# Performance work log

Measured on AMD Instinct MI355X. Metric: run time of the kernel, lower is better.

The kernel has to match this reference:

```python
import jax, jax.numpy as jnp
import numpy as np

N, E = 8192, 65536
IN_C, OUT_C, EF = 64, 16, 8
L1, L2 = 48, 32  # in - floor((in-out)/3), in - floor(2*(in-out)/3)


def setup_inputs() -> dict:
    key = jax.random.key(0)
    ks = jax.random.split(key, 10)
    rn = lambda k, shape, s: jax.random.normal(k, shape, dtype=jnp.float32) * s
    return {
        "x": jax.random.normal(ks[0], (N, IN_C), dtype=jnp.float32),
        "edge_index": jax.random.randint(ks[1], (2, E), 0, N, dtype=jnp.int32),
        "edge_attr": jax.random.normal(ks[2], (E, EF), dtype=jnp.float32),
        "nn1_w": rn(ks[3], (EF, IN_C * L1), 0.05),
        "nn1_b": jnp.zeros((IN_C * L1,), jnp.float32),
        "root1": rn(ks[4], (IN_C, L1), 0.1),
        "bias1": jnp.zeros((L1,), jnp.float32),
        "nn2_w": rn(ks[5], (EF, L1 * L2), 0.05),
        "nn2_b": jnp.zeros((L1 * L2,), jnp.float32),
        "root2": rn(ks[6], (L1, L2), 0.1),
        "bias2": jnp.zeros((L2,), jnp.float32),
        "mu_w": rn(ks[7], (L2, OUT_C), 0.1),
        "mu_b": jnp.zeros((OUT_C,), jnp.float32),
        "ls_w": rn(ks[8], (L2, OUT_C), 0.1),
        "ls_b": jnp.zeros((OUT_C,), jnp.float32),
    }


def _nnconv(x, src, dst, edge_attr, nn_w, nn_b, root, bias, c_in, c_out):
    # edge MLP -> per-edge weight matrices [E, c_in, c_out]
    w = (edge_attr @ nn_w + nn_b).reshape(-1, c_in, c_out)
    msg = jnp.einsum('ei,eio->eo', x[src], w)  # gather + per-edge matvec
    agg = jax.ops.segment_sum(msg, dst, num_segments=x.shape[0])  # sum aggregation
    return agg + x @ root + bias  # root transform + bias


def _gcn(x, src, dst, w, b):
    n = x.shape[0]
    # degree over target nodes, including self-loop (edge_weight = 1)
    deg = jax.ops.segment_sum(jnp.ones_like(src, jnp.float32), dst, num_segments=n) + 1.0
    dinv = jax.lax.rsqrt(deg)
    h = x @ w
    norm = dinv[src] * dinv[dst]  # [E]
    agg = jax.ops.segment_sum(h[src] * norm[:, None], dst, num_segments=n)
    return agg + h * (1.0 / deg)[:, None] + b  # self-loop contribution: deg_i^{-1}


def reference(x, edge_index, edge_attr, nn1_w, nn1_b, root1, bias1,
              nn2_w, nn2_b, root2, bias2, mu_w, mu_b, ls_w, ls_b):
    src, dst = edge_index[0], edge_index[1]
    h = jax.nn.relu(_nnconv(x, src, dst, edge_attr, nn1_w, nn1_b, root1, bias1, IN_C, L1))
    h = jax.nn.relu(_nnconv(h, src, dst, edge_attr, nn2_w, nn2_b, root2, bias2, L1, L2))
    return (_gcn(h, src, dst, mu_w, mu_b), _gcn(h, src, dst, ls_w, ls_b))
```

## Files before the change

kernel.cpp:

```cpp
#include <hip/hip_runtime.h>

#define NN 8192
#define EE 65536
#define K1 640
#define K2 480
#define ZS1 652
#define ZS2 492


__global__ __launch_bounds__(256) void k_zero(int* __restrict__ p) {
    int i = blockIdx.x * 256 + threadIdx.x;
    ((int4*)p)[i] = make_int4(0, 0, 0, 0);
}

__global__ __launch_bounds__(256) void k_count(const int* __restrict__ ei,
                                               int* __restrict__ cnt) {
    int e = blockIdx.x * 256 + threadIdx.x;
    if (e < EE) atomicAdd(&cnt[ei[EE + e]], 1);
}

__global__ __launch_bounds__(256) void k_scan(const int* __restrict__ cnt,
                                              int* __restrict__ rowstart,
                                              int* __restrict__ cursor) {
    __shared__ int part[256];
    const int t = threadIdx.x;
    const int base = t * 32;
    int local[32];
    int sum = 0;
#pragma unroll
    for (int k = 0; k < 32; k++) { local[k] = cnt[base + k]; sum += local[k]; }
    part[t] = sum;
    __syncthreads();
    if (t == 0) {
        int run = 0;
        for (int i = 0; i < 256; i++) { int c = part[i]; part[i] = run; run += c; }
    }
    __syncthreads();
    int run = part[t];
#pragma unroll
    for (int k = 0; k < 32; k++) {
        rowstart[base + k] = run;
        cursor[base + k] = run;
        run += local[k];
    }
    if (t == 255) rowstart[NN] = run;
}

__global__ __launch_bounds__(256) void k_scatter(const int* __restrict__ ei,
                                                 const float* __restrict__ ea,
                                                 int* __restrict__ cursor,
                                                 int* __restrict__ ssrc,
                                                 float* __restrict__ sea) {
    int e = blockIdx.x * 256 + threadIdx.x;
    if (e >= EE) return;
    int s = ei[e], d = ei[EE + e];
    int pos = atomicAdd(&cursor[d], 1);
    ssrc[pos] = s;
    const float4* a = (const float4*)(ea + (size_t)e * 8);
    float4* bp = (float4*)(sea + (size_t)pos * 8);
    bp[0] = a[0];
    bp[1] = a[1];
}

__global__ __launch_bounds__(256) void k_L1(const int* __restrict__ rowstart,
                                            const int* __restrict__ ssrc,
                                            const float* __restrict__ sea,
                                            const float* __restrict__ x,
                                            const float* __restrict__ nn1_w,
                                            const float* __restrict__ nn1_b,
                                            const float* __restrict__ root1,
                                            const float* __restrict__ bias1,
                                            float* __restrict__ h1) {
    __shared__ __align__(16) float Zt[8 * ZS1];
    __shared__ __align__(16) float Ws[64 * 48];
    __shared__ float pacc[8][8][48];
    const int n0 = blockIdx.x * 8;
    {
        const int wv = threadIdx.x >> 6;
        const int i = threadIdx.x & 63;
        const int nnA = wv * 2, nnB = nnA + 1;
        int jA = rowstart[n0 + nnA], eA = rowstart[n0 + nnA + 1];
        int jB = rowstart[n0 + nnB], eB = rowstart[n0 + nnB + 1];
        float aA[8] = {0, 0, 0, 0, 0, 0, 0, 0}, sA = 0.f;
        float aB[8] = {0, 0, 0, 0, 0, 0, 0, 0}, sB = 0.f;
        while (jA < eA || jB < eB) {
            int cjA[8], cjB[8];
#pragma unroll
            for (int p = 0; p < 8; p++) {
                int ja = jA + p; cjA[p] = (ja < eA) ? ja : 0;
                int jb = jB + p; cjB[p] = (jb < eB) ? jb : 0;
            }
            int sjA[8], sjB[8];
#pragma unroll
            for (int p = 0; p < 8; p++) { sjA[p] = ssrc[cjA[p]]; sjB[p] = ssrc[cjB[p]]; }
            float xvA[8], xvB[8];
#pragma unroll
            for (int p = 0; p < 8; p++) {
                xvA[p] = x[(size_t)sjA[p] * 64 + i];
                xvB[p] = x[(size_t)sjB[p] * 64 + i];
            }
#pragma unroll
            for (int p = 0; p < 8; p++) {
                {
                    const float4* q4 = (const float4*)(sea + (size_t)cjA[p] * 8);
                    float4 e0 = q4[0], e1 = q4[1];
                    float xx = (jA + p < eA) ? xvA[p] : 0.f;
                    aA[0] += e0.x * xx; aA[1] += e0.y * xx; aA[2] += e0.z * xx; aA[3] += e0.w * xx;
                    aA[4] += e1.x * xx; aA[5] += e1.y * xx; aA[6] += e1.z * xx; aA[7] += e1.w * xx;
                    sA += xx;
                }
                {
                    const float4* q4 = (const float4*)(sea + (size_t)cjB[p] * 8);
                    float4 e0 = q4[0], e1 = q4[1];
                    float xx = (jB + p < eB) ? xvB[p] : 0.f;
                    aB[0] += e0.x * xx; aB[1] += e0.y * xx; aB[2] += e0.z * xx; aB[3] += e0.w * xx;
                    aB[4] += e1.x * xx; aB[5] += e1.y * xx; aB[6] += e1.z * xx; aB[7] += e1.w * xx;
                    sB += xx;
                }
            }
            jA += 8; jB += 8;
        }
        float* zrA = Zt + nnA * ZS1;
        float* zrB = Zt + nnB * ZS1;
#pragma unroll
        for (int f = 0; f < 8; f++) { zrA[f * 64 + i] = aA[f]; zrB[f * 64 + i] = aB[f]; }
        zrA[512 + i] = sA; zrB[512 + i] = sB;
        zrA[576 + i] = x[(size_t)(n0 + nnA) * 64 + i];
        zrB[576 + i] = x[(size_t)(n0 + nnB) * 64 + i];
    }
    const int o  = threadIdx.x & 15;
    const int q  = (threadIdx.x >> 4) & 1;
    const int ks = threadIdx.x >> 5;
    float acc[4][3];
#pragma unroll
    for (int m = 0; m < 4; m++)
#pragma unroll
        for (int cc = 0; cc < 3; cc++) acc[m][cc] = 0.f;
    for (int c = 0; c < 10; ++c) {
        __syncthreads();
        const float* src = (c < 8) ? nn1_w + c * 3072 : (c == 8 ? nn1_b : root1);
#pragma unroll
        for (int i2 = 0; i2 < 3; i2++) {
            int g = threadIdx.x + i2 * 256;
            *(float4*)&Ws[g * 4] = *(const float4*)&src[g * 4];
        }
        __syncthreads();
        const int kl0 = ks * 8;
        const int kg0 = c * 64 + kl0;
#pragma unroll
        for (int kk = 0; kk < 8; kk += 4) {
            const int kl = kl0 + kk, kg = kg0 + kk;
            float zc[4][4];
#pragma unroll
            for (int m = 0; m < 4; m++) {
                float4 z = *(const float4*)&Zt[(q * 4 + m) * ZS1 + kg];
                zc[m][0] = z.x; zc[m][1] = z.y; zc[m][2] = z.z; zc[m][3] = z.w;
            }
#pragma unroll
            for (int dk = 0; dk < 4; dk++) {
                float w0 = Ws[(kl + dk) * 48 + o];
                float w1 = Ws[(kl + dk) * 48 + o + 16];
                float w2 = Ws[(kl + dk) * 48 + o + 32];
#pragma unroll
                for (int m = 0; m < 4; m++) {
                    acc[m][0] += zc[m][dk] * w0;
                    acc[m][1] += zc[m][dk] * w1;
                    acc[m][2] += zc[m][dk] * w2;
                }
            }
        }
    }
#pragma unroll
    for (int m = 0; m < 4; m++) {
        pacc[ks][q * 4 + m][o]      = acc[m][0];
        pacc[ks][q * 4 + m][o + 16] = acc[m][1];
        pacc[ks][q * 4 + m][o + 32] = acc[m][2];
    }
    __syncthreads();
    for (int r = threadIdx.x; r < 8 * 48; r += 256) {
        int nn = r / 48, oc = r - nn * 48;
        float v = bias1[oc];
#pragma unroll
        for (int k = 0; k < 8; k++) v += pacc[k][nn][oc];
        h1[(size_t)(n0 + nn) * 48 + oc] = v > 0.f ? v : 0.f;
    }
}

__global__ __launch_bounds__(256) void k_L2(const int* __restrict__ rowstart,
                                            const int* __restrict__ ssrc,
                                            const float* __restrict__ sea,
                                            const float* __restrict__ h1,
                                            const float* __restrict__ nn2_w,
                                            const float* __restrict__ nn2_b,
                                            const float* __restrict__ root2,
                                            const float* __restrict__ bias2,
                                            const float* __restrict__ mu_w,
                                            const float* __restrict__ mu_b,
                                            const float* __restrict__ ls_w,
                                            const float* __restrict__ ls_b,
                                            float* __restrict__ hmu,
                                            float* __restrict__ hls,
                                            float* __restrict__ dinv,
                                            float* __restrict__ out) {
    __shared__ __align__(16) float Zt[8 * ZS2];
    __shared__ __align__(16) float Ws[96 * 32];
    __shared__ float pacc[8][8][32];
    __shared__ float h2s[8][33];
    const int n0 = blockIdx.x * 8;
    {
        const int wv = threadIdx.x >> 6;
        const int i = threadIdx.x & 63;
        if (i < 48) {
            const int nnA = wv * 2, nnB = nnA + 1;
            int jA = rowstart[n0 + nnA], eA = rowstart[n0 + nnA + 1];
            int jB = rowstart[n0 + nnB], eB = rowstart[n0 + nnB + 1];
            float aA[8] = {0, 0, 0, 0, 0, 0, 0, 0}, sA = 0.f;
            float aB[8] = {0, 0, 0, 0, 0, 0, 0, 0}, sB = 0.f;
            while (jA < eA || jB < eB) {
                int cjA[8], cjB[8];
#pragma unroll
                for (int p = 0; p < 8; p++) {
                    int ja = jA + p; cjA[p] = (ja < eA) ? ja : 0;
                    int jb = jB + p; cjB[p] = (jb < eB) ? jb : 0;
                }
                int sjA[8], sjB[8];
#pragma unroll
                for (int p = 0; p < 8; p++) { sjA[p] = ssrc[cjA[p]]; sjB[p] = ssrc[cjB[p]]; }
                float hvA[8], hvB[8];
#pragma unroll
                for (int p = 0; p < 8; p++) {
                    hvA[p] = h1[(size_t)sjA[p] * 48 + i];
                    hvB[p] = h1[(size_t)sjB[p] * 48 + i];
                }
#pragma unroll
                for (int p = 0; p < 8; p++) {
                    {
                        const float4* q4 = (const float4*)(sea + (size_t)cjA[p] * 8);
                        float4 e0 = q4[0], e1 = q4[1];
                        float xx = (jA + p < eA) ? hvA[p] : 0.f;
                        aA[0] += e0.x * xx; aA[1] += e0.y * xx; aA[2] += e0.z * xx; aA[3] += e0.w * xx;
                        aA[4] += e1.x * xx; aA[5] += e1.y * xx; aA[6] += e1.z * xx; aA[7] += e1.w * xx;
                        sA += xx;
                    }
                    {
                        const float4* q4 = (const float4*)(sea + (size_t)cjB[p] * 8);
                        float4 e0 = q4[0], e1 = q4[1];
                        float xx = (jB + p < eB) ? hvB[p] : 0.f;
                        aB[0] += e0.x * xx; aB[1] += e0.y * xx; aB[2] += e0.z * xx; aB[3] += e0.w * xx;
                        aB[4] += e1.x * xx; aB[5] += e1.y * xx; aB[6] += e1.z * xx; aB[7] += e1.w * xx;
                        sB += xx;
                    }
                }
                jA += 8; jB += 8;
            }
            float* zrA = Zt + nnA * ZS2;
            float* zrB = Zt + nnB * ZS2;
#pragma unroll
            for (int f = 0; f < 8; f++) { zrA[f * 48 + i] = aA[f]; zrB[f * 48 + i] = aB[f]; }
            zrA[384 + i] = sA; zrB[384 + i] = sB;
            zrA[432 + i] = h1[(size_t)(n0 + nnA) * 48 + i];
            zrB[432 + i] = h1[(size_t)(n0 + nnB) * 48 + i];
        }
    }
    const int o  = threadIdx.x & 15;
    const int q  = (threadIdx.x >> 4) & 1;
    const int ks = threadIdx.x >> 5;
    float acc[4][2];
#pragma unroll
    for (int m = 0; m < 4; m++) { acc[m][0] = 0.f; acc[m][1] = 0.f; }
    for (int c = 0; c < 5; ++c) {
        __syncthreads();
#pragma unroll
        for (int i2 = 0; i2 < 3; i2++) {
            int g = threadIdx.x + i2 * 256;
            const float* s4;
            if (c < 4)          s4 = nn2_w + c * 3072 + g * 4;
            else if (g < 384)   s4 = nn2_b + g * 4;
            else                s4 = root2 + (g - 384) * 4;
            *(float4*)&Ws[g * 4] = *(const float4*)s4;
        }
        __syncthreads();
        const int kl0 = ks * 12;
        const int kg0 = c * 96 + kl0;
#pragma unroll
        for (int kk = 0; kk < 12; kk += 4) {
            const int kl = kl0 + kk, kg = kg0 + kk;
            float zc[4][4];
#pragma unroll
            for (int m = 0; m < 4; m++) {
                float4 z = *(const float4*)&Zt[(q * 4 + m) * ZS2 + kg];
                zc[m][0] = z.x; zc[m][1] = z.y; zc[m][2] = z.z; zc[m][3] = z.w;
            }
#pragma unroll
            for (int dk = 0; dk < 4; dk++) {
                float w0 = Ws[(kl + dk) * 32 + o];
                float w1 = Ws[(kl + dk) * 32 + o + 16];
#pragma unroll
                for (int m = 0; m < 4; m++) {
                    acc[m][0] += zc[m][dk] * w0;
                    acc[m][1] += zc[m][dk] * w1;
                }
            }
        }
    }
#pragma unroll
    for (int m = 0; m < 4; m++) {
        pacc[ks][q * 4 + m][o]      = acc[m][0];
        pacc[ks][q * 4 + m][o + 16] = acc[m][1];
    }
    __syncthreads();
    {
        int nn = threadIdx.x >> 5, oc = threadIdx.x & 31;
        float v = bias2[oc];
#pragma unroll
        for (int k = 0; k < 8; k++) v += pacc[k][nn][oc];
        h2s[nn][oc] = v > 0.f ? v : 0.f;
    }
    __syncthreads();
    if (threadIdx.x < 128) {
        const int oc = threadIdx.x & 15;
        const int nn = threadIdx.x >> 4;
        const int gn = n0 + nn;
        float am = 0.f, al = 0.f;
#pragma unroll
        for (int i = 0; i < 32; i++) {
            float hv = h2s[nn][i];
            am += hv * mu_w[i * 16 + oc];
            al += hv * ls_w[i * 16 + oc];
        }
        float d = (float)(rowstart[gn + 1] - rowstart[gn]) + 1.0f;
        float di = rsqrtf(d);
        if (oc == 0) dinv[gn] = di;
        hmu[(size_t)gn * 16 + oc] = am;
        hls[(size_t)gn * 16 + oc] = al;
        out[(size_t)gn * 16 + oc] = am / d + mu_b[oc];
        out[(size_t)NN * 16 + (size_t)gn * 16 + oc] = al / d + ls_b[oc];
    }
}

__global__ __launch_bounds__(256) void k_gcn(const int* __restrict__ rowstart,
                                             const int* __restrict__ ssrc,
                                             const float* __restrict__ hmu,
                                             const float* __restrict__ hls,
                                             const float* __restrict__ dinv,
                                             float* __restrict__ out) {
    const int wave = threadIdx.x >> 6;
    const int lane = threadIdx.x & 63;
    const int o = lane & 15, p = lane >> 4;
    const int d = blockIdx.x * 4 + wave;
    const int rs = rowstart[d], re = rowstart[d + 1];
    float am = 0.f, al = 0.f;
    for (int j = rs + p; j < re; j += 4) {
        int s = ssrc[j];
        float ds_ = dinv[s];
        am += hmu[(size_t)s * 16 + o] * ds_;
        al += hls[(size_t)s * 16 + o] * ds_;
    }
    am += __shfl_xor(am, 16); al += __shfl_xor(al, 16);
    am += __shfl_xor(am, 32); al += __shfl_xor(al, 32);
    if (p == 0) {
        float dd = dinv[d];
        out[(size_t)d * 16 + o] += am * dd;
        out[(size_t)NN * 16 + (size_t)d * 16 + o] += al * dd;
    }
}

extern "C" void kernel_launch(void* const* d_in, const int* in_sizes, int n_in,
                              void* d_out, int out_size, void* d_ws, size_t ws_size,
                              hipStream_t stream) {
    const float* x     = (const float*)d_in[0];
    const int*   ei    = (const int*)d_in[1];
    const float* ea    = (const float*)d_in[2];
    const float* nn1_w = (const float*)d_in[3];
    const float* nn1_b = (const float*)d_in[4];
    const float* root1 = (const float*)d_in[5];
    const float* bias1 = (const float*)d_in[6];
    const float* nn2_w = (const float*)d_in[7];
    const float* nn2_b = (const float*)d_in[8];
    const float* root2 = (const float*)d_in[9];
    const float* bias2 = (const float*)d_in[10];
    const float* mu_w  = (const float*)d_in[11];
    const float* mu_b  = (const float*)d_in[12];
    const float* ls_w  = (const float*)d_in[13];
    const float* ls_b  = (const float*)d_in[14];
    float* out = (float*)d_out;

    float* W    = (float*)d_ws;
    float* sea  = W;
    float* h1   = sea + 524288;
    float* hmu  = h1 + 393216;
    float* hls  = hmu + 131072;
    float* dinv = hls + 131072;
    int* cnt      = (int*)(dinv + 8192);
    int* rowstart = cnt + 8192;
    int* cursor   = rowstart + 8193;
    int* ssrc     = cursor + 8192;

    k_zero<<<dim3(8), dim3(256), 0, stream>>>(cnt);
    k_count<<<dim3(EE / 256), dim3(256), 0, stream>>>(ei, cnt);
    k_scan<<<dim3(1), dim3(256), 0, stream>>>(cnt, rowstart, cursor);
    k_scatter<<<dim3(EE / 256), dim3(256), 0, stream>>>(ei, ea, cursor, ssrc, sea);
    k_L1<<<dim3(NN / 8), dim3(256), 0, stream>>>(rowstart, ssrc, sea, x,
                                                 nn1_w, nn1_b, root1, bias1, h1);
    k_L2<<<dim3(NN / 8), dim3(256), 0, stream>>>(rowstart, ssrc, sea, h1,
                                                 nn2_w, nn2_b, root2, bias2,
                                                 mu_w, mu_b, ls_w, ls_b,
                                                 hmu, hls, dinv, out);
    k_gcn<<<dim3(NN / 4), dim3(256), 0, stream>>>(rowstart, ssrc,
                                                  hmu, hls, dinv, out);
}
```

Before: 154.6 us.

## Fuse all stages into one persistent cooperative kernel with grid syncs

Replaces the seven separate kernel launches (zero, count, scan, scatter, layer1, layer2, gcn) with a single cooperative persistent kernel. Stages are separated by grid.sync and loop over node tiles with a grid sized from occupancy. Shared memory is merged into one reused buffer, and the GCN stage now maps 8 nodes per block with 2 edge lanes per output. The aim is to remove launch overhead and inter-kernel gaps. In exchange it adds grid-wide barrier costs, runs the serial scan on a single block while the others wait, and may lower occupancy in the heavy layer stages.

After: 536.7 us. 3.47x slower.

```diff
diff --git a/kernel.cpp b/kernel.cpp
--- a/kernel.cpp
+++ b/kernel.cpp
@@ -1,367 +1,363 @@
 #include <hip/hip_runtime.h>
+#include <hip/hip_cooperative_groups.h>
+
+namespace cg = cooperative_groups;
 
 #define NN 8192
 #define EE 65536
-#define K1 640
-#define K2 480
+#define NTILE 1024
 #define ZS1 652
 #define ZS2 492
-
-
-__global__ __launch_bounds__(256) void k_zero(int* __restrict__ p) {
-    int i = blockIdx.x * 256 + threadIdx.x;
-    ((int4*)p)[i] = make_int4(0, 0, 0, 0);
-}
-
-__global__ __launch_bounds__(256) void k_count(const int* __restrict__ ei,
-                                               int* __restrict__ cnt) {
-    int e = blockIdx.x * 256 + threadIdx.x;
-    if (e < EE) atomicAdd(&cnt[ei[EE + e]], 1);
-}
-
-__global__ __launch_bounds__(256) void k_scan(const int* __restrict__ cnt,
-                                              int* __restrict__ rowstart,
-                                              int* __restrict__ cursor) {
-    __shared__ int part[256];
-    const int t = threadIdx.x;
-    const int base = t * 32;
-    int local[32];
-    int sum = 0;
-#pragma unroll
-    for (int k = 0; k < 32; k++) { local[k] = cnt[base + k]; sum += local[k]; }
-    part[t] = sum;
-    __syncthreads();
-    if (t == 0) {
-        int run = 0;
-        for (int i = 0; i < 256; i++) { int c = part[i]; part[i] = run; run += c; }
-    }
-    __syncthreads();
-    int run = part[t];
-#pragma unroll
-    for (int k = 0; k < 32; k++) {
-        rowstart[base + k] = run;
-        cursor[base + k] = run;
-        run += local[k];
-    }
-    if (t == 255) rowstart[NN] = run;
-}
-
-__global__ __launch_bounds__(256) void k_scatter(const int* __restrict__ ei,
-                                                 const float* __restrict__ ea,
-                                                 int* __restrict__ cursor,
-                                                 int* __restrict__ ssrc,
-                                                 float* __restrict__ sea) {
-    int e = blockIdx.x * 256 + threadIdx.x;
-    if (e >= EE) return;
-    int s = ei[e], d = ei[EE + e];
-    int pos = atomicAdd(&cursor[d], 1);
-    ssrc[pos] = s;
-    const float4* a = (const float4*)(ea + (size_t)e * 8);
-    float4* bp = (float4*)(sea + (size_t)pos * 8);
-    bp[0] = a[0];
-    bp[1] = a[1];
-}
-
-__global__ __launch_bounds__(256) void k_L1(const int* __restrict__ rowstart,
-                                            const int* __restrict__ ssrc,
-                                            const float* __restrict__ sea,
-                                            const float* __restrict__ x,
-                                            const float* __restrict__ nn1_w,
-                                            const float* __restrict__ nn1_b,
-                                            const float* __restrict__ root1,
-                                            const float* __restrict__ bias1,
-                                            float* __restrict__ h1) {
-    __shared__ __align__(16) float Zt[8 * ZS1];
-    __shared__ __align__(16) float Ws[64 * 48];
-    __shared__ float pacc[8][8][48];
-    const int n0 = blockIdx.x * 8;
+#define U_OFF 5216
+#define SMEM_FLOATS (U_OFF + 3072)
+
+__global__ __launch_bounds__(256, 4) void k_all(
+    const float* __restrict__ x, const int* __restrict__ ei,
+    const float* __restrict__ ea,
+    const float* __restrict__ nn1_w, const float* __restrict__ nn1_b,
+    const float* __restrict__ root1, const float* __restrict__ bias1,
+    const float* __restrict__ nn2_w, const float* __restrict__ nn2_b,
+    const float* __restrict__ root2, const float* __restrict__ bias2,
+    const float* __restrict__ mu_w, const float* __restrict__ mu_b,
+    const float* __restrict__ ls_w, const float* __restrict__ ls_b,
+    float* out, float* ws) {
+    cg::grid_group grid = cg::this_grid();
+    __shared__ __align__(16) float smem[SMEM_FLOATS];
+
+    float* sea  = ws;
+    float* h1   = sea + 524288;
+    float* hmu  = h1 + 393216;
+    float* hls  = hmu + 131072;
+    float* dinv = hls + 131072;
+    int* cnt      = (int*)(dinv + 8192);
+    int* rowstart = cnt + 8192;
+    int* cursor   = rowstart + 8193;
+    int* ssrc     = cursor + 8192;
+
+    const int tid = blockIdx.x * 256 + threadIdx.x;
+    const int nthreads = gridDim.x * 256;
+
+    for (int i = tid; i < 2048; i += nthreads)
+        ((int4*)cnt)[i] = make_int4(0, 0, 0, 0);
+    grid.sync();
+
+    for (int e = tid; e < EE; e += nthreads)
+        atomicAdd(&cnt[ei[EE + e]], 1);
+    grid.sync();
+
+    if (blockIdx.x == 0) {
+        int* part = (int*)smem;
+        const int t = threadIdx.x;
+        const int base = t * 32;
+        int local[32];
+        int sum = 0;
+#pragma unroll
+        for (int k = 0; k < 32; k++) { local[k] = cnt[base + k]; sum += local[k]; }
+        part[t] = sum;
+        __syncthreads();
+        if (t == 0) {
+            int run = 0;
+            for (int i = 0; i < 256; i++) { int c = part[i]; part[i] = run; run += c; }
+        }
+        __syncthreads();
+        int run = part[t];
+#pragma unroll
+        for (int k = 0; k < 32; k++) {
+            rowstart[base + k] = run;
+            cursor[base + k] = run;
+            run += local[k];
+        }
+        if (t == 255) rowstart[NN] = run;
+    }
+    grid.sync();
+
+    for (int e = tid; e < EE; e += nthreads) {
+        int s = ei[e], d = ei[EE + e];
+        int pos = atomicAdd(&cursor[d], 1);
+        ssrc[pos] = s;
+        const float4* a = (const float4*)(ea + (size_t)e * 8);
+        float4* bp = (float4*)(sea + (size_t)pos * 8);
+        bp[0] = a[0];
+        bp[1] = a[1];
+    }
+    grid.sync();
+
     {
-        const int wv = threadIdx.x >> 6;
-        const int i = threadIdx.x & 63;
-        const int nnA = wv * 2, nnB = nnA + 1;
-        int jA = rowstart[n0 + nnA], eA = rowstart[n0 + nnA + 1];
-        int jB = rowstart[n0 + nnB], eB = rowstart[n0 + nnB + 1];
-        float aA[8] = {0, 0, 0, 0, 0, 0, 0, 0}, sA = 0.f;
-        float aB[8] = {0, 0, 0, 0, 0, 0, 0, 0}, sB = 0.f;
-        while (jA < eA || jB < eB) {
-            int cjA[8], cjB[8];
-#pragma unroll
-            for (int p = 0; p < 8; p++) {
-                int ja = jA + p; cjA[p] = (ja < eA) ? ja : 0;
-                int jb = jB + p; cjB[p] = (jb < eB) ? jb : 0;
-            }
-            int sjA[8], sjB[8];
-#pragma unroll
-            for (int p = 0; p < 8; p++) { sjA[p] = ssrc[cjA[p]]; sjB[p] = ssrc[cjB[p]]; }
-            float xvA[8], xvB[8];
-#pragma unroll
-            for (int p = 0; p < 8; p++) {
-                xvA[p] = x[(size_t)sjA[p] * 64 + i];
-                xvB[p] = x[(size_t)sjB[p] * 64 + i];
-            }
-#pragma unroll
-            for (int p = 0; p < 8; p++) {
-                {
-                    const float4* q4 = (const float4*)(sea + (size_t)cjA[p] * 8);
-                    float4 e0 = q4[0], e1 = q4[1];
-                    float xx = (jA + p < eA) ? xvA[p] : 0.f;
-                    aA[0] += e0.x * xx; aA[1] += e0.y * xx; aA[2] += e0.z * xx; aA[3] += e0.w * xx;
-                    aA[4] += e1.x * xx; aA[5] += e1.y * xx; aA[6] += e1.z * xx; aA[7] += e1.w * xx;
-                    sA += xx;
-                }
-                {
-                    const float4* q4 = (const float4*)(sea + (size_t)cjB[p] * 8);
-                    float4 e0 = q4[0], e1 = q4[1];
-                    float xx = (jB + p < eB) ? xvB[p] : 0.f;
-                    aB[0] += e0.x * xx; aB[1] += e0.y * xx; aB[2] += e0.z * xx; aB[3] += e0.w * xx;
-                    aB[4] += e1.x * xx; aB[5] += e1.y * xx; aB[6] += e1.z * xx; aB[7] += e1.w * xx;
-                    sB += xx;
-                }
-            }
-            jA += 8; jB += 8;
-        }
-        float* zrA = Zt + nnA * ZS1;
-        float* zrB = Zt + nnB * ZS1;
-#pragma unroll
-        for (int f = 0; f < 8; f++) { zrA[f * 64 + i] = aA[f]; zrB[f * 64 + i] = aB[f]; }
-        zrA[512 + i] = sA; zrB[512 + i] = sB;
-        zrA[576 + i] = x[(size_t)(n0 + nnA) * 64 + i];
-        zrB[576 + i] = x[(size_t)(n0 + nnB) * 64 + i];
-    }
-    const int o  = threadIdx.x & 15;
-    const int q  = (threadIdx.x >> 4) & 1;
-    const int ks = threadIdx.x >> 5;
-    float acc[4][3];
-#pragma unroll
-    for (int m = 0; m < 4; m++)
-#pragma unroll
-        for (int cc = 0; cc < 3; cc++) acc[m][cc] = 0.f;
-    for (int c = 0; c < 10; ++c) {
-        __syncthreads();
-        const float* src = (c < 8) ? nn1_w + c * 3072 : (c == 8 ? nn1_b : root1);
-#pragma unroll
-        for (int i2 = 0; i2 < 3; i2++) {
-            int g = threadIdx.x + i2 * 256;
-            *(float4*)&Ws[g * 4] = *(const float4*)&src[g * 4];
-        }
-        __syncthreads();
-        const int kl0 = ks * 8;
-        const int kg0 = c * 64 + kl0;
-#pragma unroll
-        for (int kk = 0; kk < 8; kk += 4) {
-            const int kl = kl0 + kk, kg = kg0 + kk;
-            float zc[4][4];
+        float* Zt = smem;
+        float* U  = smem + U_OFF;
+        for (int tile = blockIdx.x; tile < NTILE; tile += gridDim.x) {
+            const int n0 = tile * 8;
+            {
+                const int wv = threadIdx.x >> 6;
+                const int i = threadIdx.x & 63;
+                const int nnA = wv * 2, nnB = nnA + 1;
+                int jA = rowstart[n0 + nnA], eA = rowstart[n0 + nnA + 1];
+                int jB = rowstart[n0 + nnB], eB = rowstart[n0 + nnB + 1];
+                float aA[8] = {0, 0, 0, 0, 0, 0, 0, 0}, sA = 0.f;
+                float aB[8] = {0, 0, 0, 0, 0, 0, 0, 0}, sB = 0.f;
+                while (jA < eA || jB < eB) {
+                    int cjA[8], cjB[8];
+#pragma unroll
+                    for (int p = 0; p < 8; p++) {
+                        int ja = jA + p; cjA[p] = (ja < eA) ? ja : 0;
+                        int jb = jB + p; cjB[p] = (jb < eB) ? jb : 0;
+                    }
+                    int sjA[8], sjB[8];
+#pragma unroll
+                    for (int p = 0; p < 8; p++) { sjA[p] = ssrc[cjA[p]]; sjB[p] = ssrc[cjB[p]]; }
+                    float xvA[8], xvB[8];
+#pragma unroll
+                    for (int p = 0; p < 8; p++) {
+                        xvA[p] = x[(size_t)sjA[p] * 64 + i];
+                        xvB[p] = x[(size_t)sjB[p] * 64 + i];
+                    }
+#pragma unroll
+                    for (int p = 0; p < 8; p++) {
+                        {
+                            const float4* q4 = (const float4*)(sea + (size_t)cjA[p] * 8);
+                            float4 e0 = q4[0], e1 = q4[1];
+                            float xx = (jA + p < eA) ? xvA[p] : 0.f;
+                            aA[0] += e0.x * xx; aA[1] += e0.y * xx; aA[2] += e0.z * xx; aA[3] += e0.w * xx;
+                            aA[4] += e1.x * xx; aA[5] += e1.y * xx; aA[6] += e1.z * xx; aA[7] += e1.w * xx;
+                            sA += xx;
+                        }
+                        {
+                            const float4* q4 = (const float4*)(sea + (size_t)cjB[p] * 8);
+                            float4 e0 = q4[0], e1 = q4[1];
+                            float xx = (jB + p < eB) ? xvB[p] : 0.f;
+                            aB[0] += e0.x * xx; aB[1] += e0.y * xx; aB[2] += e0.z * xx; aB[3] += e0.w * xx;
+                            aB[4] += e1.x * xx; aB[5] += e1.y * xx; aB[6] += e1.z * xx; aB[7] += e1.w * xx;
+                            sB += xx;
+                        }
+                    }
+                    jA += 8; jB += 8;
+                }
+                float* zrA = Zt + nnA * ZS1;
+                float* zrB = Zt + nnB * ZS1;
+#pragma unroll
+                for (int f = 0; f < 8; f++) { zrA[f * 64 + i] = aA[f]; zrB[f * 64 + i] = aB[f]; }
+                zrA[512 + i] = sA; zrB[512 + i] = sB;
+                zrA[576 + i] = x[(size_t)(n0 + nnA) * 64 + i];
+                zrB[576 + i] = x[(size_t)(n0 + nnB) * 64 + i];
+            }
+            const int o  = threadIdx.x & 15;
+            const int q  = (threadIdx.x >> 4) & 1;
+            const int ks = threadIdx.x >> 5;
+            float acc[4][3];
+#pragma unroll
+            for (int m = 0; m < 4; m++)
+#pragma unroll
+                for (int cc = 0; cc < 3; cc++) acc[m][cc] = 0.f;
+            for (int c = 0; c < 10; ++c) {
+                __syncthreads();
+                const float* src = (c < 8) ? nn1_w + c * 3072 : (c == 8 ? nn1_b : root1);
+#pragma unroll
+                for (int i2 = 0; i2 < 3; i2++) {
+                    int g = threadIdx.x + i2 * 256;
+                    *(float4*)&U[g * 4] = *(const float4*)&src[g * 4];
+                }
+                __syncthreads();
+                const int kl0 = ks * 8;
+                const int kg0 = c * 64 + kl0;
+#pragma unroll
+                for (int kk = 0; kk < 8; kk += 4) {
+                    const int kl = kl0 + kk, kg = kg0 + kk;
+                    float zc[4][4];
+#pragma unroll
+                    for (int m = 0; m < 4; m++) {
+                        float4 z = *(const float4*)&Zt[(q * 4 + m) * ZS1 + kg];
+                        zc[m][0] = z.x; zc[m][1] = z.y; zc[m][2] = z.z; zc[m][3] = z.w;
+                    }
+#pragma unroll
+                    for (int dk = 0; dk < 4; dk++) {
+                        float w0 = U[(kl + dk) * 48 + o];
+                        float w1 = U[(kl + dk) * 48 + o + 16];
+                        float w2 = U[(kl + dk) * 48 + o + 32];
+#pragma unroll
+                        for (int m = 0; m < 4; m++) {
+                            acc[m][0] += zc[m][dk] * w0;
+                            acc[m][1] += zc[m][dk] * w1;
+                            acc[m][2] += zc[m][dk] * w2;
+                        }
+                    }
+                }
+            }
+            __syncthreads();
 #pragma unroll
             for (int m = 0; m < 4; m++) {
-                float4 z = *(const float4*)&Zt[(q * 4 + m) * ZS1 + kg];
-                zc[m][0] = z.x; zc[m][1] = z.y; zc[m][2] = z.z; zc[m][3] = z.w;
-            }
-#pragma unroll
-            for (int dk = 0; dk < 4; dk++) {
-                float w0 = Ws[(kl + dk) * 48 + o];
-                float w1 = Ws[(kl + dk) * 48 + o + 16];
-                float w2 = Ws[(kl + dk) * 48 + o + 32];
-#pragma unroll
-                for (int m = 0; m < 4; m++) {
-                    acc[m][0] += zc[m][dk] * w0;
-                    acc[m][1] += zc[m][dk] * w1;
-                    acc[m][2] += zc[m][dk] * w2;
-                }
-            }
-        }
-    }
-#pragma unroll
-    for (int m = 0; m < 4; m++) {
-        pacc[ks][q * 4 + m][o]      = acc[m][0];
-        pacc[ks][q * 4 + m][o + 16] = acc[m][1];
-        pacc[ks][q * 4 + m][o + 32] = acc[m][2];
-    }
-    __syncthreads();
-    for (int r = threadIdx.x; r < 8 * 48; r += 256) {
-        int nn = r / 48, oc = r - nn * 48;
-        float v = bias1[oc];
-#pragma unroll
-        for (int k = 0; k < 8; k++) v += pacc[k][nn][oc];
-        h1[(size_t)(n0 + nn) * 48 + oc] = v > 0.f ? v : 0.f;
-    }
-}
-
-__global__ __launch_bounds__(256) void k_L2(const int* __restrict__ rowstart,
-                                            const int* __restrict__ ssrc,
-                                            const float* __restrict__ sea,
-                                            const float* __restrict__ h1,
-                                            const float* __restrict__ nn2_w,
-                                            const float* __restrict__ nn2_b,
-                                            const float* __restrict__ root2,
-                                            const float* __restrict__ bias2,
-                                            const float* __restrict__ mu_w,
-                                            const float* __restrict__ mu_b,
-                                            const float* __restrict__ ls_w,
-                                            const float* __restrict__ ls_b,
-                                            float* __restrict__ hmu,
-                                            float* __restrict__ hls,
-                                            float* __restrict__ dinv,
-                                            float* __restrict__ out) {
-    __shared__ __align__(16) float Zt[8 * ZS2];
-    __shared__ __align__(16) float Ws[96 * 32];
-    __shared__ float pacc[8][8][32];
-    __shared__ float h2s[8][33];
-    const int n0 = blockIdx.x * 8;
+                U[(ks * 8 + q * 4 + m) * 48 + o]      = acc[m][0];
+                U[(ks * 8 + q * 4 + m) * 48 + o + 16] = acc[m][1];
+                U[(ks * 8 + q * 4 + m) * 48 + o + 32] = acc[m][2];
+            }
+            __syncthreads();
+            for (int r = threadIdx.x; r < 8 * 48; r += 256) {
+                int nn = r / 48, oc = r - nn * 48;
+                float v = bias1[oc];
+#pragma unroll
+                for (int k = 0; k < 8; k++) v += U[(k * 8 + nn) * 48 + oc];
+                h1[(size_t)(n0 + nn) * 48 + oc] = v > 0.f ? v : 0.f;
+            }
+        }
+    }
+    grid.sync();
+
     {
-        const int wv = threadIdx.x >> 6;
-        const int i = threadIdx.x & 63;
-        if (i < 48) {
-            const int nnA = wv * 2, nnB = nnA + 1;
-            int jA = rowstart[n0 + nnA], eA = rowstart[n0 + nnA + 1];
-            int jB = rowstart[n0 + nnB], eB = rowstart[n0 + nnB + 1];
-            float aA[8] = {0, 0, 0, 0, 0, 0, 0, 0}, sA = 0.f;
-            float aB[8] = {0, 0, 0, 0, 0, 0, 0, 0}, sB = 0.f;
-            while (jA < eA || jB < eB) {
-                int cjA[8], cjB[8];
-#pragma unroll
-                for (int p = 0; p < 8; p++) {
-                    int ja = jA + p; cjA[p] = (ja < eA) ? ja : 0;
-                    int jb = jB + p; cjB[p] = (jb < eB) ? jb : 0;
-                }
-                int sjA[8], sjB[8];
-#pragma unroll
-                for (int p = 0; p < 8; p++) { sjA[p] = ssrc[cjA[p]]; sjB[p] = ssrc[cjB[p]]; }
-                float hvA[8], hvB[8];
-#pragma unroll
-                for (int p = 0; p < 8; p++) {
-                    hvA[p] = h1[(size_t)sjA[p] * 48 + i];
-                    hvB[p] = h1[(size_t)sjB[p] * 48 + i];
-                }
-#pragma unroll
-                for (int p = 0; p < 8; p++) {
-                    {
-                        const float4* q4 = (const float4*)(sea + (size_t)cjA[p] * 8);
-                        float4 e0 = q4[0], e1 = q4[1];
-                        float xx = (jA + p < eA) ? hvA[p] : 0.f;
-                        aA[0] += e0.x * xx; aA[1] += e0.y * xx; aA[2] += e0.z * xx; aA[3] += e0.w * xx;
-                        aA[4] += e1.x * xx; aA[5] += e1.y * xx; aA[6] += e1.z * xx; aA[7] += e1.w * xx;
-                        sA += xx;
-                    }
-                    {
-                        const float4* q4 = (const float4*)(sea + (size_t)cjB[p] * 8);
-                        float4 e0 = q4[0], e1 = q4[1];
-                        float xx = (jB + p < eB) ? hvB[p] : 0.f;
-                        aB[0] += e0.x * xx; aB[1] += e0.y * xx; aB[2] += e0.z * xx; aB[3] += e0.w * xx;
-                        aB[4] += e1.x * xx; aB[5] += e1.y * xx; aB[6] += e1.z * xx; aB[7] += e1.w * xx;
-                        sB += xx;
-                    }
-                }
-                jA += 8; jB += 8;
-            }
-            float* zrA = Zt + nnA * ZS2;
-            float* zrB = Zt + nnB * ZS2;
-#pragma unroll
-            for (int f = 0; f < 8; f++) { zrA[f * 48 + i] = aA[f]; zrB[f * 48 + i] = aB[f]; }
-            zrA[384 + i] = sA; zrB[384 + i] = sB;
-            zrA[432 + i] = h1[(size_t)(n0 + nnA) * 48 + i];
-            zrB[432 + i] = h1[(size_t)(n0 + nnB) * 48 + i];
-        }
-    }
-    const int o  = threadIdx.x & 15;
-    const int q  = (threadIdx.x >> 4) & 1;
-    const int ks = threadIdx.x >> 5;
-    float acc[4][2];
-#pragma unroll
-    for (int m = 0; m < 4; m++) { acc[m][0] = 0.f; acc[m][1] = 0.f; }
-    for (int c = 0; c < 5; ++c) {
-        __syncthreads();
-#pragma unroll
-        for (int i2 = 0; i2 < 3; i2++) {
-            int g = threadIdx.x + i2 * 256;
-            const float* s4;
-            if (c < 4)          s4 = nn2_w + c * 3072 + g * 4;
-            else if (g < 384)   s4 = nn2_b + g * 4;
-            else                s4 = root2 + (g - 384) * 4;
-            *(float4*)&Ws[g * 4] = *(const float4*)s4;
-        }
-        __syncthreads();
-        const int kl0 = ks * 12;
-        const int kg0 = c * 96 + kl0;
-#pragma unroll
-        for (int kk = 0; kk < 12; kk += 4) {
-            const int kl = kl0 + kk, kg = kg0 + kk;
-            float zc[4][4];
+        float* Zt = smem;
+        float* U  = smem + U_OFF;
+        for (int tile = blockIdx.x; tile < NTILE; tile += gridDim.x) {
+            const int n0 = tile * 8;
+            {
+                const int wv = threadIdx.x >> 6;
+                const int i = threadIdx.x & 63;
+                if (i < 48) {
+                    const int nnA = wv * 2, nnB = nnA + 1;
+                    int jA = rowstart[n0 + nnA], eA = rowstart[n0 + nnA + 1];
+                    int jB = rowstart[n0 + nnB], eB = rowstart[n0 + nnB + 1];
+                    float aA[8] = {0, 0, 0, 0, 0, 0, 0, 0}, sA = 0.f;
+                    float aB[8] = {0, 0, 0, 0, 0, 0, 0, 0}, sB = 0.f;
+                    while (jA < eA || jB < eB) {
+                        int cjA[8], cjB[8];
+#pragma unroll
+                        for (int p = 0; p < 8; p++) {
+                            int ja = jA + p; cjA[p] = (ja < eA) ? ja : 0;
+                            int jb = jB + p; cjB[p] = (jb < eB) ? jb : 0;
+                        }
+                        int sjA[8], sjB[8];
+#pragma unroll
+                        for (int p = 0; p < 8; p++) { sjA[p] = ssrc[cjA[p]]; sjB[p] = ssrc[cjB[p]]; }
+                        float hvA[8], hvB[8];
+#pragma unroll
+                        for (int p = 0; p < 8; p++) {
+                            hvA[p] = h1[(size_t)sjA[p] * 48 + i];
+                            hvB[p] = h1[(size_t)sjB[p] * 48 + i];
+                        }
+#pragma unroll
+                        for (int p = 0; p < 8; p++) {
+                            {
+                                const float4* q4 = (const float4*)(sea + (size_t)cjA[p] * 8);
+                                float4 e0 = q4[0], e1 = q4[1];
+                                float xx = (jA + p < eA) ? hvA[p] : 0.f;
+                                aA[0] += e0.x * xx; aA[1] += e0.y * xx; aA[2] += e0.z * xx; aA[3] += e0.w * xx;
+                                aA[4] += e1.x * xx; aA[5] += e1.y * xx; aA[6] += e1.z * xx; aA[7] += e1.w * xx;
+                                sA += xx;
+                            }
+                            {
+                                const float4* q4 = (const float4*)(sea + (size_t)cjB[p] * 8);
+                                float4 e0 = q4[0], e1 = q4[1];
+                                float xx = (jB + p < eB) ? hvB[p] : 0.f;
+                                aB[0] += e0.x * xx; aB[1] += e0.y * xx; aB[2] += e0.z * xx; aB[3] += e0.w * xx;
+                                aB[4] += e1.x * xx; aB[5] += e1.y * xx; aB[6] += e1.z * xx; aB[7] += e1.w * xx;
+                                sB += xx;
+                            }
+                        }
+                        jA += 8; jB += 8;
+                    }
+                    float* zrA = Zt + nnA * ZS2;
+                    float* zrB = Zt + nnB * ZS2;
+#pragma unroll
+                    for (int f = 0; f < 8; f++) { zrA[f * 48 + i] = aA[f]; zrB[f * 48 + i] = aB[f]; }
+                    zrA[384 + i] = sA; zrB[384 + i] = sB;
+                    zrA[432 + i] = h1[(size_t)(n0 + nnA) * 48 + i];
+                    zrB[432 + i] = h1[(size_t)(n0 + nnB) * 48 + i];
+                }
+            }
+            const int o  = threadIdx.x & 15;
+            const int q  = (threadIdx.x >> 4) & 1;
+            const int ks = threadIdx.x >> 5;
+            float acc[4][2];
+#pragma unroll
+            for (int m = 0; m < 4; m++) { acc[m][0] = 0.f; acc[m][1] = 0.f; }
+            for (int c = 0; c < 5; ++c) {
+                __syncthreads();
+#pragma unroll
+                for (int i2 = 0; i2 < 3; i2++) {
+                    int g = threadIdx.x + i2 * 256;
+                    const float* s4;
+                    if (c < 4)        s4 = nn2_w + c * 3072 + g * 4;
+                    else if (g < 384) s4 = nn2_b + g * 4;
+                    else              s4 = root2 + (g - 384) * 4;
+                    *(float4*)&U[g * 4] = *(const float4*)s4;
+                }
+                __syncthreads();
+                const int kl0 = ks * 12;
+                const int kg0 = c * 96 + kl0;
+#pragma unroll
+                for (int kk = 0; kk < 12; kk += 4) {
+                    const int kl = kl0 + kk, kg = kg0 + kk;
+                    float zc[4][4];
+#pragma unroll
+                    for (int m = 0; m < 4; m++) {
+                        float4 z = *(const float4*)&Zt[(q * 4 + m) * ZS2 + kg];
+                        zc[m][0] = z.x; zc[m][1] = z.y; zc[m][2] = z.z; zc[m][3] = z.w;
+                    }
+#pragma unroll
+                    for (int dk = 0; dk < 4; dk++) {
+                        float w0 = U[(kl + dk) * 32 + o];
+                        float w1 = U[(kl + dk) * 32 + o + 16];
+#pragma unroll
+                        for (int m = 0; m < 4; m++) {
+                            acc[m][0] += zc[m][dk] * w0;
+                            acc[m][1] += zc[m][dk] * w1;
+                        }
+                    }
+                }
+            }
+            __syncthreads();
 #pragma unroll
             for (int m = 0; m < 4; m++) {
-                float4 z = *(const float4*)&Zt[(q * 4 + m) * ZS2 + kg];
-                zc[m][0] = z.x; zc[m][1] = z.y; zc[m][2] = z.z; zc[m][3] = z.w;
-            }
-#pragma unroll
-            for (int dk = 0; dk < 4; dk++) {
-                float w0 = Ws[(kl + dk) * 32 + o];
-                float w1 = Ws[(kl + dk) * 32 + o + 16];
-#pragma unroll
-                for (int m = 0; m < 4; m++) {
-                    acc[m][0] += zc[m][dk] * w0;
-                    acc[m][1] += zc[m][dk] * w1;
-                }
-            }
-        }
-    }
-#pragma unroll
-    for (int m = 0; m < 4; m++) {
-        pacc[ks][q * 4 + m][o]      = acc[m][0];
-        pacc[ks][q * 4 + m][o + 16] = acc[m][1];
-    }
-    __syncthreads();
-    {
-        int nn = threadIdx.x >> 5, oc = threadIdx.x & 31;
-        float v = bias2[oc];
-#pragma unroll
-        for (int k = 0; k < 8; k++) v += pacc[k][nn][oc];
-        h2s[nn][oc] = v > 0.f ? v : 0.f;
-    }
-    __syncthreads();
-    if (threadIdx.x < 128) {
-        const int oc = threadIdx.x & 15;
-        const int nn = threadIdx.x >> 4;
-        const int gn = n0 + nn;
+                U[(ks * 8 + q * 4 + m) * 32 + o]      = acc[m][0];
+                U[(ks * 8 + q * 4 + m) * 32 + o + 16] = acc[m][1];
+            }
+            __syncthreads();
+            {
+                int nn = threadIdx.x >> 5, oc = threadIdx.x & 31;
+                float v = bias2[oc];
+#pragma unroll
+                for (int k = 0; k < 8; k++) v += U[(k * 8 + nn) * 32 + oc];
+                U[2048 + nn * 33 + oc] = v > 0.f ? v : 0.f;
+            }
+            __syncthreads();
+            if (threadIdx.x < 128) {
+                const int oc = threadIdx.x & 15;
+                const int nn = threadIdx.x >> 4;
+                const int gn = n0 + nn;
+                float am = 0.f, al = 0.f;
+#pragma unroll
+                for (int i = 0; i < 32; i++) {
+                    float hv = U[2048 + nn * 33 + i];
+                    am += hv * mu_w[i * 16 + oc];
+                    al += hv * ls_w[i * 16 + oc];
+                }
+                float d = (float)(rowstart[gn + 1] - rowstart[gn]) + 1.0f;
+                float di = rsqrtf(d);
+                if (oc == 0) dinv[gn] = di;
+                hmu[(size_t)gn * 16 + oc] = am;
+                hls[(size_t)gn * 16 + oc] = al;
+                out[(size_t)gn * 16 + oc] = am / d + mu_b[oc];
+                out[(size_t)NN * 16 + (size_t)gn * 16 + oc] = al / d + ls_b[oc];
+            }
+        }
+    }
+    grid.sync();
+
+    for (int nb = blockIdx.x; nb < NTILE; nb += gridDim.x) {
+        const int node = nb * 8 + (threadIdx.x >> 5);
+        const int o = threadIdx.x & 15;
+        const int p = (threadIdx.x >> 4) & 1;
+        const int rs = rowstart[node], re = rowstart[node + 1];
         float am = 0.f, al = 0.f;
-#pragma unroll
-        for (int i = 0; i < 32; i++) {
-            float hv = h2s[nn][i];
-            am += hv * mu_w[i * 16 + oc];
-            al += hv * ls_w[i * 16 + oc];
-        }
-        float d = (float)(rowstart[gn + 1] - rowstart[gn]) + 1.0f;
-        float di = rsqrtf(d);
-        if (oc == 0) dinv[gn] = di;
-        hmu[(size_t)gn * 16 + oc] = am;
-        hls[(size_t)gn * 16 + oc] = al;
-        out[(size_t)gn * 16 + oc] = am / d + mu_b[oc];
-        out[(size_t)NN * 16 + (size_t)gn * 16 + oc] = al / d + ls_b[oc];
-    }
-}
-
-__global__ __launch_bounds__(256) void k_gcn(const int* __restrict__ rowstart,
-                                             const int* __restrict__ ssrc,
-                                             const float* __restrict__ hmu,
-                                             const float* __restrict__ hls,
-                                             const float* __restrict__ dinv,
-                                             float* __restrict__ out) {
-    const int wave = threadIdx.x >> 6;
-    const int lane = threadIdx.x & 63;
-    const int o = lane & 15, p = lane >> 4;
-    const int d = blockIdx.x * 4 + wave;
-    const int rs = rowstart[d], re = rowstart[d + 1];
-    float am = 0.f, al = 0.f;
-    for (int j = rs + p; j < re; j += 4) {
-        int s = ssrc[j];
-        float ds_ = dinv[s];
-        am += hmu[(size_t)s * 16 + o] * ds_;
-        al += hls[(size_t)s * 16 + o] * ds_;
-    }
-    am += __shfl_xor(am, 16); al += __shfl_xor(al, 16);
-    am += __shfl_xor(am, 32); al += __shfl_xor(al, 32);
-    if (p == 0) {
-        float dd = dinv[d];
-        out[(size_t)d * 16 + o] += am * dd;
-        out[(size_t)NN * 16 + (size_t)d * 16 + o] += al * dd;
+        for (int j = rs + p; j < re; j += 2) {
+            int s = ssrc[j];
+            float ds_ = dinv[s];
+            am += hmu[(size_t)s * 16 + o] * ds_;
+            al += hls[(size_t)s * 16 + o] * ds_;
+        }
+        am += __shfl_xor(am, 16); al += __shfl_xor(al, 16);
+        if (p == 0) {
+            float dd = dinv[node];
+            out[(size_t)node * 16 + o] += am * dd;
+            out[(size_t)NN * 16 + (size_t)node * 16 + o] += al * dd;
+        }
     }
 }
 
@@ -384,28 +380,23 @@
     const float* ls_w  = (const float*)d_in[13];
     const float* ls_b  = (const float*)d_in[14];
     float* out = (float*)d_out;
-
-    float* W    = (float*)d_ws;
-    float* sea  = W;
-    float* h1   = sea + 524288;
-    float* hmu  = h1 + 393216;
-    float* hls  = hmu + 131072;
-    float* dinv = hls + 131072;
-    int* cnt      = (int*)(dinv + 8192);
-    int* rowstart = cnt + 8192;
-    int* cursor   = rowstart + 8193;
-    int* ssrc     = cursor + 8192;
-
-    k_zero<<<dim3(8), dim3(256), 0, stream>>>(cnt);
-    k_count<<<dim3(EE / 256), dim3(256), 0, stream>>>(ei, cnt);
-    k_scan<<<dim3(1), dim3(256), 0, stream>>>(cnt, rowstart, cursor);
-    k_scatter<<<dim3(EE / 256), dim3(256), 0, stream>>>(ei, ea, cursor, ssrc, sea);
-    k_L1<<<dim3(NN / 8), dim3(256), 0, stream>>>(rowstart, ssrc, sea, x,
-                                                 nn1_w, nn1_b, root1, bias1, h1);
-    k_L2<<<dim3(NN / 8), dim3(256), 0, stream>>>(rowstart, ssrc, sea, h1,
-                                                 nn2_w, nn2_b, root2, bias2,
-                                                 mu_w, mu_b, ls_w, ls_b,
-                                                 hmu, hls, dinv, out);
-    k_gcn<<<dim3(NN / 4), dim3(256), 0, stream>>>(rowstart, ssrc,
-                                                  hmu, hls, dinv, out);
+    float* ws  = (float*)d_ws;
+
+    static int gridBlocks = 0;
+    if (gridBlocks == 0) {
+        int nb = 0;
+        hipError_t err = hipOccupancyMaxActiveBlocksPerMultiprocessor(&nb, k_all, 256, 0);
+        if (err != hipSuccess || nb < 1) nb = 1;
+        long g = (long)nb * 256;
+        if (g > NTILE) g = NTILE;
+        gridBlocks = (int)g;
+    }
+
+    void* args[] = {(void*)&x,     (void*)&ei,    (void*)&ea,
+                    (void*)&nn1_w, (void*)&nn1_b, (void*)&root1, (void*)&bias1,
+                    (void*)&nn2_w, (void*)&nn2_b, (void*)&root2, (void*)&bias2,
+                    (void*)&mu_w,  (void*)&mu_b,  (void*)&ls_w,  (void*)&ls_b,
+                    (void*)&out,   (void*)&ws};
+    hipLaunchCooperativeKernel((const void*)k_all, dim3(gridBlocks), dim3(256),
+                               args, 0, stream);
 }
```
